# Optimization experiments

Hardware: AMD Instinct MI355X
Metric: run time of the kernel (lower is better)

## Reference

```python
import jax, jax.numpy as jnp
import numpy as np
import math

B, L, DIM, DEPTH, HEADS, DH, T, BUCKETS, MAXDIST = 256, 77, 768, 12, 12, 64, 1000, 32, 128
INNER = HEADS * DH            # 768
FF_IN = 4 * DIM               # 3072 (SwiGLU inner)
EPS = 1e-5


def rmsnorm(x, gamma):
    inv = jax.lax.rsqrt(jnp.sum(x * x, axis=-1, keepdims=True) + EPS)
    return x * inv * gamma * (DIM ** 0.5)


def rel_pos_bias(i, j, table):
    # table: [BUCKETS, HEADS] -> bias [HEADS, i, j]
    q_pos = jnp.arange(i)
    k_pos = jnp.arange(j)
    rel = k_pos[None, :] - q_pos[:, None]
    n = jnp.maximum(-rel, 0)
    max_exact = BUCKETS // 2
    is_small = n < max_exact
    nf = jnp.maximum(n, 1).astype(jnp.float32)
    val_large = max_exact + (jnp.log(nf / max_exact) / math.log(MAXDIST / max_exact) * (BUCKETS - max_exact)).astype(jnp.int32)
    val_large = jnp.minimum(val_large, BUCKETS - 1)
    bucket = jnp.where(is_small, n, val_large)
    return jnp.transpose(table[bucket], (2, 0, 1))  # h i j


def attention(x, mask, bias, gamma, Wq, Wkv, Wout, null_kv):
    b, n, _ = x.shape
    xn = rmsnorm(x, gamma)
    q = (xn @ Wq).reshape(b, n, HEADS, DH).transpose(0, 2, 1, 3)     # b h n d
    kv = xn @ Wkv                                                     # b n 2d (single head)
    k, v = kv[..., :DH], kv[..., DH:]
    nk = jnp.broadcast_to(null_kv[0], (b, 1, DH))
    nv = jnp.broadcast_to(null_kv[1], (b, 1, DH))
    k = jnp.concatenate([nk, k], axis=1)                              # b (n+1) d
    v = jnp.concatenate([nv, v], axis=1)
    sim = jnp.einsum('bhid,bjd->bhij', q * (DH ** -0.5), k) + bias[None]
    neg = -jnp.finfo(sim.dtype).max
    m = jnp.pad(mask, ((0, 0), (1, 0)), constant_values=True)         # null kv always visible
    sim = jnp.where(m[:, None, None, :], sim, neg)
    i, j = n, n + 1
    causal = jnp.arange(j)[None, :] > (jnp.arange(i)[:, None] + (j - i))
    sim = jnp.where(causal[None, None], neg, sim)
    attn = jax.nn.softmax(sim - jax.lax.stop_gradient(sim.max(axis=-1, keepdims=True)), axis=-1)
    out = jnp.einsum('bhij,bjd->bhid', attn, v)
    out = out.transpose(0, 2, 1, 3).reshape(b, n, INNER)
    return out @ Wout


def feedforward(x, gamma, W1, W2):
    h = rmsnorm(x, gamma) @ W1                                        # b n 2*FF_IN
    a, gate = h[..., :FF_IN], h[..., FF_IN:]
    return (a * jax.nn.silu(gate)) @ W2


def setup_inputs() -> dict:
    key = jax.random.key(0)
    ks = jax.random.split(key, 16)
    s = 0.02
    return {
        'image_embed': jax.random.normal(ks[0], (B, DIM), jnp.float32),
        'text_encodings': jax.random.normal(ks[1], (B, L, DIM), jnp.float32),
        'text_embed': jax.random.normal(ks[2], (B, DIM), jnp.float32),
        'time_emb_table': jax.random.normal(ks[3], (T, DIM), jnp.float32) * s,
        'learned_query': jax.random.normal(ks[4], (DIM,), jnp.float32),
        'rel_bias_table': jax.random.normal(ks[5], (BUCKETS, HEADS), jnp.float32) * s,
        'attn_gamma': jnp.ones((DEPTH, DIM), jnp.float32),
        'Wq': jax.random.normal(ks[6], (DEPTH, DIM, INNER), jnp.float32) * s,
        'Wkv': jax.random.normal(ks[7], (DEPTH, DIM, 2 * DH), jnp.float32) * s,
        'Wout': jax.random.normal(ks[8], (DEPTH, INNER, DIM), jnp.float32) * s,
        'null_kv': jax.random.normal(ks[9], (DEPTH, 2, DH), jnp.float32),
        'ff_gamma': jnp.ones((DEPTH, DIM), jnp.float32),
        'Wff1': jax.random.normal(ks[10], (DEPTH, DIM, 2 * FF_IN), jnp.float32) * s,
        'Wff2': jax.random.normal(ks[11], (DEPTH, FF_IN, DIM), jnp.float32) * s,
        'diffusion_timesteps': jax.random.randint(ks[12], (B,), 0, T),
        'mask': jnp.ones((B, L), dtype=bool),
    }


def reference(image_embed, text_encodings, text_embed, time_emb_table, learned_query,
              rel_bias_table, attn_gamma, Wq, Wkv, Wout, null_kv, ff_gamma, Wff1, Wff2,
              diffusion_timesteps, mask):
    b = image_embed.shape[0]
    # mask bookkeeping (matches torch forward); cond_drop_prob fixed at 1.0 -> keep all
    not_all = jnp.any(mask, axis=-1)
    m = jnp.concatenate([mask, not_all[:, None]], axis=1)
    m = jnp.pad(m, ((0, 0), (0, 2)), constant_values=True)            # [b, L+3]
    time_embed = time_emb_table[diffusion_timesteps][:, None, :]
    queries = jnp.broadcast_to(learned_query, (b, 1, DIM))
    tokens = jnp.concatenate([text_encodings, text_embed[:, None, :], time_embed, queries], axis=1)
    n = tokens.shape[1]
    bias = rel_pos_bias(n, n + 1, rel_bias_table)
    x = tokens
    for l in range(DEPTH):
        x = attention(x, m, bias, attn_gamma[l], Wq[l], Wkv[l], Wout[l], null_kv[l]) + x
        x = feedforward(x, ff_gamma[l], Wff1[l], Wff2[l]) + x
    return x[:, -1, :]
```

## Files before the change

### kernel.cpp

```cpp
#include <hip/hip_runtime.h>
#include <hip/hip_bf16.h>
#include <float.h>
#include <math.h>

#define NB 256
#define LTXT 77
#define DIM 768
#define DEPTH 12
#define HEADS 12
#define DH 64
#define NTOK 80
#define NKEY 81
#define NROWS (NB*NTOK)
#define FFH 3072
#define FF2C 6144
#define INNER 768
#define SROW 100

typedef __hip_bfloat16 bf16;
typedef __attribute__((ext_vector_type(8))) short short8;
typedef __attribute__((ext_vector_type(4))) float f32x4;

#define BARRIER() asm volatile("s_barrier" ::: "memory")
#define WAITV(n)  asm volatile("s_waitcnt vmcnt(" #n ")" ::: "memory")

__device__ __forceinline__ unsigned short f2bf(float f) {
    __hip_bfloat16 h = __float2bfloat16(f);
    return __builtin_bit_cast(unsigned short, h);
}

__global__ void build_tokens(const float* __restrict__ text_enc,
                             const float* __restrict__ text_emb,
                             const float* __restrict__ time_tab,
                             const float* __restrict__ lquery,
                             const int* __restrict__ tsteps,
                             float* __restrict__ x) {
    int idx = blockIdx.x * 256 + threadIdx.x;
    if (idx >= NROWS * DIM) return;
    int d = idx % DIM;
    int row = idx / DIM;
    int b = row / NTOK, p = row % NTOK;
    float v;
    if (p < LTXT)            v = text_enc[((size_t)b * LTXT + p) * DIM + d];
    else if (p == LTXT)      v = text_emb[(size_t)b * DIM + d];
    else if (p == LTXT + 1)  v = time_tab[(size_t)tsteps[b] * DIM + d];
    else                     v = lquery[d];
    x[idx] = v;
}

__global__ void build_biasR(const float* __restrict__ table, float* __restrict__ biasR) {
    int idx = blockIdx.x * 256 + threadIdx.x;
    if (idx >= HEADS * NTOK * 96) return;
    int kap = idx % 96;
    int i = (idx / 96) % NTOK;
    int h = idx / (96 * NTOK);
    float v;
    if ((kap < 80 && kap > i) || kap > 80) {
        v = -1e30f;
    } else {
        int j = (kap < 80) ? kap + 1 : 0;
        int rel = j - i;
        int n = rel < 0 ? -rel : 0;
        int bucket;
        if (n < 16) {
            bucket = n;
        } else {
            float val = logf((float)n / 16.0f) / logf(8.0f) * 16.0f;
            int vl = 16 + (int)val;
            bucket = vl < 31 ? vl : 31;
        }
        v = table[bucket * HEADS + h];
    }
    biasR[idx] = v;
}

__global__ __launch_bounds__(256) void convT(const float* __restrict__ W,
                                             bf16* __restrict__ WT,
                                             int K, int N) {
    __shared__ float t[32][33];
    int n0 = blockIdx.x * 32, k0 = blockIdx.y * 32;
    int tx = threadIdx.x & 31, ty = threadIdx.x >> 5;
    #pragma unroll
    for (int i = 0; i < 4; i++)
        t[ty + 8 * i][tx] = W[(size_t)(k0 + ty + 8 * i) * N + n0 + tx];
    __syncthreads();
    #pragma unroll
    for (int i = 0; i < 4; i++)
        WT[(size_t)(n0 + ty + 8 * i) * K + k0 + tx] = __float2bfloat16(t[tx][ty + 8 * i]);
}

__global__ __launch_bounds__(256) void rmsnorm_w(const float* __restrict__ x,
                                                 const float* __restrict__ gamma,
                                                 bf16* __restrict__ out) {
    int wave = blockIdx.x * 4 + (threadIdx.x >> 6);
    int lane = threadIdx.x & 63;
    float4 g0 = *(const float4*)&gamma[lane * 4];
    float4 g1 = *(const float4*)&gamma[lane * 4 + 256];
    float4 g2 = *(const float4*)&gamma[lane * 4 + 512];
    #pragma unroll 2
    for (int rr = 0; rr < 8; ++rr) {
        int row = wave * 8 + rr;
        const float* xr = x + (size_t)row * DIM + lane * 4;
        float4 v0 = *(const float4*)xr;
        float4 v1 = *(const float4*)(xr + 256);
        float4 v2 = *(const float4*)(xr + 512);
        float ss = v0.x*v0.x + v0.y*v0.y + v0.z*v0.z + v0.w*v0.w
                 + v1.x*v1.x + v1.y*v1.y + v1.z*v1.z + v1.w*v1.w
                 + v2.x*v2.x + v2.y*v2.y + v2.z*v2.z + v2.w*v2.w;
        #pragma unroll
        for (int o = 32; o > 0; o >>= 1) ss += __shfl_xor(ss, o);
        float inv = 27.712812921102035f / sqrtf(ss + 1e-5f);
        bf16* orow = out + (size_t)row * DIM + lane * 4;
        ushort4 w0 = { f2bf(v0.x*inv*g0.x), f2bf(v0.y*inv*g0.y), f2bf(v0.z*inv*g0.z), f2bf(v0.w*inv*g0.w) };
        ushort4 w1 = { f2bf(v1.x*inv*g1.x), f2bf(v1.y*inv*g1.y), f2bf(v1.z*inv*g1.z), f2bf(v1.w*inv*g1.w) };
        ushort4 w2 = { f2bf(v2.x*inv*g2.x), f2bf(v2.y*inv*g2.y), f2bf(v2.z*inv*g2.z), f2bf(v2.w*inv*g2.w) };
        *(ushort4*)(orow)       = w0;
        *(ushort4*)(orow + 256) = w1;
        *(ushort4*)(orow + 512) = w2;
    }
}


#define GSTAGE_N(nld, lds, base, b0, ld, kk0)                                  \
    _Pragma("unroll")                                                          \
    for (int r_ = 0; r_ < (nld); ++r_) {                                       \
        int idx_ = r_ * 256 + t;                                               \
        int row_ = idx_ >> 3, c_ = idx_ & 7;                                   \
        int cs_ = c_ ^ (row_ & 7);                                             \
        __builtin_amdgcn_global_load_lds(                                      \
            (const __attribute__((address_space(1))) unsigned int*)            \
                &base[(size_t)(b0 + row_) * ld + (kk0) + cs_ * 8],             \
            (__attribute__((address_space(3))) unsigned int*)&lds[idx_ * 8],   \
            16, 0, 0);                                                         \
    }

#define FRAG_READ(dst, lds, base_row, kk)                                      \
    _Pragma("unroll")                                                          \
    for (int q_ = 0; q_ < 4; ++q_) {                                           \
        int row_ = (base_row) + q_ * 16 + fr;                                  \
        int ch_ = ((((kk) << 2) + kb) ^ (row_ & 7));                           \
        dst[q_] = *(const short8*)&lds[row_ * 64 + ch_ * 8];                   \
    }

#define FRAG_READ2(dst, lds, base_row, kk)                                     \
    _Pragma("unroll")                                                          \
    for (int q_ = 0; q_ < 2; ++q_) {                                           \
        int row_ = (base_row) + q_ * 16 + fr;                                  \
        int ch_ = ((((kk) << 2) + kb) ^ (row_ & 7));                           \
        dst[q_] = *(const short8*)&lds[row_ * 64 + ch_ * 8];                   \
    }

template<int EPI>
__global__ __launch_bounds__(256, 2) void gemm_bt(const bf16* __restrict__ A,
                                                  const bf16* __restrict__ BT,
                                                  float* __restrict__ C,
                                                  int N, int K) {
    __shared__ __align__(16) short As[2 * 128 * 64];
    __shared__ __align__(16) short Bs[2 * 128 * 64];
    const int t = threadIdx.x;
    const int lane = t & 63;
    const int wid = t >> 6;
    const int wr = wid >> 1, wc = wid & 1;
    const int fr = lane & 15;
    const int kb = lane >> 4;
    const int row0 = blockIdx.y * 128, col0 = blockIdx.x * 128;

    f32x4 acc[4][4] = {};
    const int NKT = K >> 6;

    GSTAGE_N(4, As, A, row0, K, 0)
    GSTAGE_N(4, Bs, BT, col0, K, 0)

    for (int kt = 0; kt < NKT; ++kt) {
        const short* curA = As + (kt & 1) * (128 * 64);
        const short* curB = Bs + (kt & 1) * (128 * 64);
        if (kt + 1 < NKT) {
            short* nxtA = As + ((kt + 1) & 1) * (128 * 64);
            short* nxtB = Bs + ((kt + 1) & 1) * (128 * 64);
            int k0n = (kt + 1) << 6;
            GSTAGE_N(4, nxtA, A, row0, K, k0n)
            GSTAGE_N(4, nxtB, BT, col0, K, k0n)
            WAITV(8);
        } else {
            WAITV(0);
        }
        BARRIER();
        #pragma unroll
        for (int kk = 0; kk < 2; ++kk) {
            short8 af[4], bv[4];
            FRAG_READ(af, curA, wr * 64, kk)
            FRAG_READ(bv, curB, wc * 64, kk)
            __builtin_amdgcn_s_setprio(1);
            #pragma unroll
            for (int i = 0; i < 4; ++i)
                #pragma unroll
                for (int j = 0; j < 4; ++j)
                    acc[i][j] = __builtin_amdgcn_mfma_f32_16x16x32_bf16(af[i], bv[j], acc[i][j], 0, 0, 0);
            __builtin_amdgcn_s_setprio(0);
        }
        BARRIER();
    }

    #pragma unroll
    for (int i = 0; i < 4; ++i) {
        #pragma unroll
        for (int j = 0; j < 4; ++j) {
            int row = row0 + wr * 64 + i * 16 + kb * 4;
            int col = col0 + wc * 64 + j * 16 + fr;
            #pragma unroll
            for (int r = 0; r < 4; ++r) {
                size_t o = (size_t)(row + r) * N + col;
                if (EPI == 1)      C[o] += acc[i][j][r];
                else               ((bf16*)C)[o] = __float2bfloat16(acc[i][j][r]);
            }
        }
    }
}

__global__ __launch_bounds__(256, 2) void gemm_kv(const bf16* __restrict__ A,
                                                  const bf16* __restrict__ BT,
                                                  bf16* __restrict__ kout,
                                                  bf16* __restrict__ vT) {
    __shared__ __align__(16) short As[2 * 128 * 64];
    __shared__ __align__(16) short Bs[2 * 128 * 64];
    const int t = threadIdx.x;
    const int lane = t & 63;
    const int wid = t >> 6;
    const int wr = wid >> 1, wc = wid & 1;
    const int fr = lane & 15;
    const int kb = lane >> 4;
    const int row0 = blockIdx.y * 128;
    const int K = DIM;

    f32x4 acc[4][4] = {};
    const int NKT = DIM >> 6;

    GSTAGE_N(4, As, A, row0, K, 0)
    GSTAGE_N(4, Bs, BT, 0, K, 0)

    for (int kt = 0; kt < NKT; ++kt) {
        const short* curA = As + (kt & 1) * (128 * 64);
        const short* curB = Bs + (kt & 1) * (128 * 64);
        if (kt + 1 < NKT) {
            short* nxtA = As + ((kt + 1) & 1) * (128 * 64);
            short* nxtB = Bs + ((kt + 1) & 1) * (128 * 64);
            int k0n = (kt + 1) << 6;
            GSTAGE_N(4, nxtA, A, row0, K, k0n)
            GSTAGE_N(4, nxtB, BT, 0, K, k0n)
            WAITV(8);
        } else {
            WAITV(0);
        }
        BARRIER();
        #pragma unroll
        for (int kk = 0; kk < 2; ++kk) {
            short8 af[4], bv[4];
            FRAG_READ(af, curA, wr * 64, kk)
            FRAG_READ(bv, curB, wc * 64, kk)
            __builtin_amdgcn_s_setprio(1);
            #pragma unroll
            for (int i = 0; i < 4; ++i)
                #pragma unroll
                for (int j = 0; j < 4; ++j)
                    acc[i][j] = __builtin_amdgcn_mfma_f32_16x16x32_bf16(af[i], bv[j], acc[i][j], 0, 0, 0);
            __builtin_amdgcn_s_setprio(0);
        }
        BARRIER();
    }

    #pragma unroll
    for (int i = 0; i < 4; ++i) {
        #pragma unroll
        for (int j = 0; j < 4; ++j) {
            int row = row0 + wr * 64 + i * 16 + kb * 4;
            int col = wc * 64 + j * 16 + fr;
            #pragma unroll
            for (int r = 0; r < 4; ++r) {
                int rg = row + r;
                float v = acc[i][j][r];
                if (wc == 0) {
                    kout[(size_t)rg * 64 + col] = __float2bfloat16(v);
                } else {
                    int bb = rg / NTOK, ii = rg - bb * NTOK;
                    vT[((size_t)bb * 64 + (col - 64)) * NTOK + ii] = __float2bfloat16(v);
                }
            }
        }
    }
}

__global__ __launch_bounds__(256) void attn_mfma(const bf16* __restrict__ qb,
                                                 const bf16* __restrict__ kbuf,
                                                 const bf16* __restrict__ vT,
                                                 const float* __restrict__ nullkv,
                                                 const float* __restrict__ biasR,
                                                 bf16* __restrict__ attnb) {
    const int b = blockIdx.x / HEADS;
    const int h = blockIdx.x % HEADS;
    __shared__ __align__(16) short Ks[96 * 64];
    __shared__ __align__(16) short Vt[64 * 128];
    __shared__ __align__(16) float Sls[80 * SROW];
    char* Sb = (char*)Sls;
    const int t = threadIdx.x;
    const int lane = t & 63;
    const int wid = t >> 6;
    const int g = lane >> 4;
    const int fr = lane & 15;

    for (int c = t; c < 768; c += 256) {
        int row = c >> 3, ch = c & 7;
        short8 v;
        if (row < NTOK) {
            v = *(const short8*)&kbuf[((size_t)(b * NTOK + row)) * 64 + ch * 8];
        } else if (row == NTOK) {
            #pragma unroll
            for (int e = 0; e < 8; ++e) v[e] = (short)f2bf(nullkv[ch * 8 + e]);
        } else {
            v = short8{0,0,0,0,0,0,0,0};
        }
        *(short8*)((char*)Ks + row * 128 + ((ch ^ (row & 7)) << 4)) = v;
    }
    for (int c = t; c < 1024; c += 256) {
        int d = c >> 4, ch = c & 15;
        if (ch >= 12) continue;
        short8 v;
        if (ch < 10) {
            v = *(const short8*)&vT[((size_t)b * 64 + d) * NTOK + ch * 8];
        } else if (ch == 10) {
            v = short8{0,0,0,0,0,0,0,0};
            v[0] = (short)f2bf(nullkv[64 + d]);
        } else {
            v = short8{0,0,0,0,0,0,0,0};
        }
        *(short8*)((char*)Vt + d * 256 + ((ch ^ (d & 7)) << 4)) = v;
    }
    __syncthreads();

    const bf16* qbase = qb + ((size_t)(b * NTOK)) * INNER + h * DH;
    for (int s = 0; s < 8; ++s) {
        int tt = wid + 4 * s;
        if (tt >= 30) break;
        int m = tt / 6, n = tt - 6 * m;
        f32x4 acc = {};
        #pragma unroll
        for (int kk = 0; kk < 2; ++kk) {
            short8 a = *(const short8*)&qbase[(size_t)(m * 16 + fr) * INNER + kk * 32 + g * 8];
            int krow = n * 16 + fr;
            short8 kf = *(const short8*)((const char*)Ks + krow * 128 + ((((kk << 2) + g) ^ (krow & 7)) << 4));
            acc = __builtin_amdgcn_mfma_f32_16x16x32_bf16(a, kf, acc, 0, 0, 0);
        }
        int i0 = m * 16 + g * 4;
        int kap = n * 16 + fr;
        const float* bR = biasR + ((size_t)h * NTOK + i0) * 96 + kap;
        #pragma unroll
        for (int r = 0; r < 4; ++r)
            Sls[(i0 + r) * SROW + kap] = acc[r] * 0.125f + bR[r * 96];
    }
    __syncthreads();

    for (int rr = 0; rr < 20; ++rr) {
        int row = wid + 4 * rr;
        const float* Srow = Sls + row * SROW;
        float s0 = Srow[lane];
        float s1v = Srow[64 + (lane & 31)];
        float mx = fmaxf(s0, s1v);
        #pragma unroll
        for (int o = 32; o > 0; o >>= 1) mx = fmaxf(mx, __shfl_xor(mx, o));
        float e0 = __expf(s0 - mx);
        float e1 = (lane < 32) ? __expf(s1v - mx) : 0.0f;
        float sum = e0 + e1;
        #pragma unroll
        for (int o = 32; o > 0; o >>= 1) sum += __shfl_xor(sum, o);
        float inv = 1.0f / sum;
        *(unsigned short*)(Sb + row * (SROW * 4) + lane * 2) = f2bf(e0 * inv);
        if (lane < 32)
            *(unsigned short*)(Sb + row * (SROW * 4) + 128 + lane * 2) = f2bf(e1 * inv);
    }
    __syncthreads();

    for (int s = 0; s < 5; ++s) {
        int tt = wid + 4 * s;
        int m = tt >> 2, n = tt & 3;
        f32x4 acc = {};
        #pragma unroll
        for (int kc = 0; kc < 3; ++kc) {
            short8 p = *(const short8*)(Sb + (m * 16 + fr) * (SROW * 4) + kc * 64 + g * 16);
            int drow = n * 16 + fr;
            short8 vv = *(const short8*)((const char*)Vt + drow * 256 + ((((kc << 2) + g) ^ (drow & 7)) << 4));
            acc = __builtin_amdgcn_mfma_f32_16x16x32_bf16(p, vv, acc, 0, 0, 0);
        }
        int i0 = m * 16 + g * 4;
        int d = n * 16 + fr;
        #pragma unroll
        for (int r = 0; r < 4; ++r)
            attnb[((size_t)(b * NTOK) + i0 + r) * INNER + h * DH + d] = __float2bfloat16(acc[r]);
    }
}

__global__ __launch_bounds__(256, 2) void gemm_ff1(const bf16* __restrict__ A,
                                                   const bf16* __restrict__ W1T,
                                                   bf16* __restrict__ act) {
    __shared__ __align__(16) short As[2 * 128 * 64];
    __shared__ __align__(16) short Bs1[2 * 64 * 64];
    __shared__ __align__(16) short Bs2[2 * 64 * 64];
    const int t = threadIdx.x;
    const int lane = t & 63;
    const int wid = t >> 6;
    const int wr = wid >> 1, wc = wid & 1;
    const int fr = lane & 15;
    const int kb = lane >> 4;
    const int row0 = blockIdx.y * 128, col0 = blockIdx.x * 64;
    const int K = DIM;
    const bf16* B1 = W1T;
    const bf16* B2 = W1T + (size_t)FFH * DIM;

    f32x4 acc1[4][2] = {}, acc2[4][2] = {};
    const int NKT = DIM >> 6;

    GSTAGE_N(4, As, A, row0, K, 0)
    GSTAGE_N(2, Bs1, B1, col0, K, 0)
    GSTAGE_N(2, Bs2, B2, col0, K, 0)

    for (int kt = 0; kt < NKT; ++kt) {
        const short* curA  = As  + (kt & 1) * (128 * 64);
        const short* curB1 = Bs1 + (kt & 1) * (64 * 64);
        const short* curB2 = Bs2 + (kt & 1) * (64 * 64);
        if (kt + 1 < NKT) {
            short* nxtA  = As  + ((kt + 1) & 1) * (128 * 64);
            short* nxtB1 = Bs1 + ((kt + 1) & 1) * (64 * 64);
            short* nxtB2 = Bs2 + ((kt + 1) & 1) * (64 * 64);
            int k0n = (kt + 1) << 6;
            GSTAGE_N(4, nxtA, A, row0, K, k0n)
            GSTAGE_N(2, nxtB1, B1, col0, K, k0n)
            GSTAGE_N(2, nxtB2, B2, col0, K, k0n)
            WAITV(8);
        } else {
            WAITV(0);
        }
        BARRIER();
        #pragma unroll
        for (int kk = 0; kk < 2; ++kk) {
            short8 af[4], b1v[2], b2v[2];
            FRAG_READ(af, curA, wr * 64, kk)
            FRAG_READ2(b1v, curB1, wc * 32, kk)
            FRAG_READ2(b2v, curB2, wc * 32, kk)
            __builtin_amdgcn_s_setprio(1);
            #pragma unroll
            for (int i = 0; i < 4; ++i)
                #pragma unroll
                for (int j = 0; j < 2; ++j) {
                    acc1[i][j] = __builtin_amdgcn_mfma_f32_16x16x32_bf16(af[i], b1v[j], acc1[i][j], 0, 0, 0);
                    acc2[i][j] = __builtin_amdgcn_mfma_f32_16x16x32_bf16(af[i], b2v[j], acc2[i][j], 0, 0, 0);
                }
            __builtin_amdgcn_s_setprio(0);
        }
        BARRIER();
    }

    #pragma unroll
    for (int i = 0; i < 4; ++i) {
        #pragma unroll
        for (int j = 0; j < 2; ++j) {
            int row = row0 + wr * 64 + i * 16 + kb * 4;
            int col = col0 + wc * 32 + j * 16 + fr;
            #pragma unroll
            for (int r = 0; r < 4; ++r) {
                float a = acc1[i][j][r];
                float gt = acc2[i][j][r];
                float s = a * gt / (1.0f + __expf(-gt));
                act[(size_t)(row + r) * FFH + col] = __float2bfloat16(s);
            }
        }
    }
}

__global__ void extract(const float* __restrict__ x, float* __restrict__ out) {
    int idx = blockIdx.x * 256 + threadIdx.x;
    if (idx >= NB * DIM) return;
    int b = idx / DIM, d = idx % DIM;
    out[idx] = x[((size_t)(b * NTOK + NTOK - 1)) * DIM + d];
}

extern "C" void kernel_launch(void* const* d_in, const int* in_sizes, int n_in,
                              void* d_out, int out_size, void* d_ws, size_t ws_size,
                              hipStream_t stream) {
    (void)in_sizes; (void)n_in; (void)out_size; (void)ws_size;
    const float* text_enc = (const float*)d_in[1];
    const float* text_emb = (const float*)d_in[2];
    const float* time_tab = (const float*)d_in[3];
    const float* lquery   = (const float*)d_in[4];
    const float* rel_tab  = (const float*)d_in[5];
    const float* attn_g   = (const float*)d_in[6];
    const float* Wq       = (const float*)d_in[7];
    const float* Wkv      = (const float*)d_in[8];
    const float* Wout     = (const float*)d_in[9];
    const float* null_kv  = (const float*)d_in[10];
    const float* ff_g     = (const float*)d_in[11];
    const float* Wff1     = (const float*)d_in[12];
    const float* Wff2     = (const float*)d_in[13];
    const int*   tsteps   = (const int*)d_in[14];

    char* ws = (char*)d_ws;
    float* x     = (float*)(ws);
    bf16*  xn    = (bf16*)(ws + 62914560);
    bf16*  attnb = xn;
    char*  U     = ws + 94371840;
    bf16*  qb    = (bf16*)U;
    bf16*  kbuf  = (bf16*)(U + 31457280);
    bf16*  vT    = (bf16*)(U + 34078720);
    bf16*  act   = (bf16*)U;
    float* biasR = (float*)(ws + 220200960);
    bf16*  WqT   = (bf16*)(ws + 220569600);
    bf16*  WkvT  = (bf16*)(ws + 221749248);
    bf16*  WoutT = (bf16*)(ws + 221945856);
    bf16*  Wff1T = (bf16*)(ws + 223125504);
    bf16*  Wff2T = (bf16*)(ws + 232562688);

    build_tokens<<<(NROWS * DIM + 255) / 256, 256, 0, stream>>>(text_enc, text_emb, time_tab, lquery, tsteps, x);
    build_biasR<<<(HEADS * NTOK * 96 + 255) / 256, 256, 0, stream>>>(rel_tab, biasR);

    for (int l = 0; l < DEPTH; l++) {
        convT<<<dim3(INNER / 32, DIM / 32), 256, 0, stream>>>(Wq   + (size_t)l * DIM * INNER,  WqT,   DIM,   INNER);
        convT<<<dim3((2 * DH) / 32, DIM / 32), 256, 0, stream>>>(Wkv + (size_t)l * DIM * 2 * DH, WkvT, DIM, 2 * DH);
        convT<<<dim3(DIM / 32, INNER / 32), 256, 0, stream>>>(Wout + (size_t)l * INNER * DIM,  WoutT, INNER, DIM);
        convT<<<dim3(FF2C / 32, DIM / 32), 256, 0, stream>>>(Wff1 + (size_t)l * DIM * FF2C,    Wff1T, DIM,   FF2C);
        convT<<<dim3(DIM / 32, FFH / 32), 256, 0, stream>>>(Wff2  + (size_t)l * FFH * DIM,     Wff2T, FFH,   DIM);

        rmsnorm_w<<<NROWS / (8 * 4), 256, 0, stream>>>(x, attn_g + (size_t)l * DIM, xn);
        gemm_bt<2><<<dim3(INNER / 128, NROWS / 128), 256, 0, stream>>>(xn, WqT, (float*)qb, INNER, DIM);
        gemm_kv<<<dim3(1, NROWS / 128), 256, 0, stream>>>(xn, WkvT, kbuf, vT);
        attn_mfma<<<NB * HEADS, 256, 0, stream>>>(qb, kbuf, vT, null_kv + (size_t)l * 2 * DH, biasR, attnb);
        gemm_bt<1><<<dim3(DIM / 128, NROWS / 128), 256, 0, stream>>>(attnb, WoutT, x, DIM, INNER);

        rmsnorm_w<<<NROWS / (8 * 4), 256, 0, stream>>>(x, ff_g + (size_t)l * DIM, xn);
        gemm_ff1<<<dim3(FFH / 64, NROWS / 128), 256, 0, stream>>>(xn, Wff1T, act);
        gemm_bt<1><<<dim3(DIM / 128, NROWS / 128), 256, 0, stream>>>(act, Wff2T, x, DIM, FFH);
    }

    extract<<<(NB * DIM + 255) / 256, 256, 0, stream>>>(x, (float*)d_out);
}
```

Before: 7.894 ms.

## Skip non-final-token work in last layer, fuse QKV GEMM and weight conversions

In the last layer, only the final token's row is needed after attention, so the output projection, FF norm and both FF GEMMs run on just those 256 rows using strided leading dimensions. The Q and KV projections are merged into one GEMM over a concatenated transposed weight, and the five per-layer weight transposes become one launch. This removes about a twelfth of the FF and output-projection compute plus several launches. The cost is extra stride parameters and special-case code paths.

```diff
diff --git a/kernel.cpp b/kernel.cpp
--- a/kernel.cpp
+++ b/kernel.cpp
@@ -74,19 +74,34 @@
     biasR[idx] = v;
 }
 
-__global__ __launch_bounds__(256) void convT(const float* __restrict__ W,
-                                             bf16* __restrict__ WT,
-                                             int K, int N) {
-    __shared__ float t[32][33];
-    int n0 = blockIdx.x * 32, k0 = blockIdx.y * 32;
+__global__ __launch_bounds__(256) void convT_all(const float* __restrict__ Wq,
+                                                 const float* __restrict__ Wkv,
+                                                 const float* __restrict__ Wout,
+                                                 const float* __restrict__ Wff1,
+                                                 const float* __restrict__ Wff2,
+                                                 bf16* __restrict__ WqkvT,
+                                                 bf16* __restrict__ WoutT,
+                                                 bf16* __restrict__ Wff1T,
+                                                 bf16* __restrict__ Wff2T) {
+    int bid = blockIdx.x;
+    const float* W; bf16* WT; int K, N, local;
+    if (bid < 576)       { W = Wq;   WT = WqkvT;             K = 768;  N = 768;  local = bid; }
+    else if (bid < 672)  { W = Wkv;  WT = WqkvT + 768 * 768; K = 768;  N = 128;  local = bid - 576; }
+    else if (bid < 1248) { W = Wout; WT = WoutT;             K = 768;  N = 768;  local = bid - 672; }
+    else if (bid < 5856) { W = Wff1; WT = Wff1T;             K = 768;  N = 6144; local = bid - 1248; }
+    else                 { W = Wff2; WT = Wff2T;             K = 3072; N = 768;  local = bid - 5856; }
+    int nblk = N / 32;
+    int n0 = (local % nblk) * 32, k0 = (local / nblk) * 32;
+
+    __shared__ float tt[32][33];
     int tx = threadIdx.x & 31, ty = threadIdx.x >> 5;
     #pragma unroll
     for (int i = 0; i < 4; i++)
-        t[ty + 8 * i][tx] = W[(size_t)(k0 + ty + 8 * i) * N + n0 + tx];
+        tt[ty + 8 * i][tx] = W[(size_t)(k0 + ty + 8 * i) * N + n0 + tx];
     __syncthreads();
     #pragma unroll
     for (int i = 0; i < 4; i++)
-        WT[(size_t)(n0 + ty + 8 * i) * K + k0 + tx] = __float2bfloat16(t[tx][ty + 8 * i]);
+        WT[(size_t)(n0 + ty + 8 * i) * K + k0 + tx] = __float2bfloat16(tt[tx][ty + 8 * i]);
 }
 
 __global__ __launch_bounds__(256) void rmsnorm_w(const float* __restrict__ x,
@@ -120,6 +135,37 @@
     }
 }
 
+__global__ __launch_bounds__(256) void rmsnorm_last(const float* __restrict__ x,
+                                                    const float* __restrict__ gamma,
+                                                    bf16* __restrict__ out) {
+    int wave = blockIdx.x * 4 + (threadIdx.x >> 6);
+    int lane = threadIdx.x & 63;
+    float4 g0 = *(const float4*)&gamma[lane * 4];
+    float4 g1 = *(const float4*)&gamma[lane * 4 + 256];
+    float4 g2 = *(const float4*)&gamma[lane * 4 + 512];
+    #pragma unroll 2
+    for (int rr = 0; rr < 8; ++rr) {
+        int row = wave * 8 + rr;
+        const float* xr = x + ((size_t)row * NTOK + 79) * DIM + lane * 4;
+        float4 v0 = *(const float4*)xr;
+        float4 v1 = *(const float4*)(xr + 256);
+        float4 v2 = *(const float4*)(xr + 512);
+        float ss = v0.x*v0.x + v0.y*v0.y + v0.z*v0.z + v0.w*v0.w
+                 + v1.x*v1.x + v1.y*v1.y + v1.z*v1.z + v1.w*v1.w
+                 + v2.x*v2.x + v2.y*v2.y + v2.z*v2.z + v2.w*v2.w;
+        #pragma unroll
+        for (int o = 32; o > 0; o >>= 1) ss += __shfl_xor(ss, o);
+        float inv = 27.712812921102035f / sqrtf(ss + 1e-5f);
+        bf16* orow = out + (size_t)row * DIM + lane * 4;
+        ushort4 w0 = { f2bf(v0.x*inv*g0.x), f2bf(v0.y*inv*g0.y), f2bf(v0.z*inv*g0.z), f2bf(v0.w*inv*g0.w) };
+        ushort4 w1 = { f2bf(v1.x*inv*g1.x), f2bf(v1.y*inv*g1.y), f2bf(v1.z*inv*g1.z), f2bf(v1.w*inv*g1.w) };
+        ushort4 w2 = { f2bf(v2.x*inv*g2.x), f2bf(v2.y*inv*g2.y), f2bf(v2.z*inv*g2.z), f2bf(v2.w*inv*g2.w) };
+        *(ushort4*)(orow)       = w0;
+        *(ushort4*)(orow + 256) = w1;
+        *(ushort4*)(orow + 512) = w2;
+    }
+}
+
 
 #define GSTAGE_N(nld, lds, base, b0, ld, kk0)                                  \
     _Pragma("unroll")                                                          \
@@ -129,7 +175,7 @@
         int cs_ = c_ ^ (row_ & 7);                                             \
         __builtin_amdgcn_global_load_lds(                                      \
             (const __attribute__((address_space(1))) unsigned int*)            \
-                &base[(size_t)(b0 + row_) * ld + (kk0) + cs_ * 8],             \
+                &base[(size_t)(b0 + row_) * (ld) + (kk0) + cs_ * 8],           \
             (__attribute__((address_space(3))) unsigned int*)&lds[idx_ * 8],   \
             16, 0, 0);                                                         \
     }
@@ -154,7 +200,7 @@
 __global__ __launch_bounds__(256, 2) void gemm_bt(const bf16* __restrict__ A,
                                                   const bf16* __restrict__ BT,
                                                   float* __restrict__ C,
-                                                  int N, int K) {
+                                                  int N, int K, int lda, int ldc) {
     __shared__ __align__(16) short As[2 * 128 * 64];
     __shared__ __align__(16) short Bs[2 * 128 * 64];
     const int t = threadIdx.x;
@@ -167,6 +213,73 @@
 
     f32x4 acc[4][4] = {};
     const int NKT = K >> 6;
+
+    GSTAGE_N(4, As, A, row0, lda, 0)
+    GSTAGE_N(4, Bs, BT, col0, K, 0)
+
+    for (int kt = 0; kt < NKT; ++kt) {
+        const short* curA = As + (kt & 1) * (128 * 64);
+        const short* curB = Bs + (kt & 1) * (128 * 64);
+        if (kt + 1 < NKT) {
+            short* nxtA = As + ((kt + 1) & 1) * (128 * 64);
+            short* nxtB = Bs + ((kt + 1) & 1) * (128 * 64);
+            int k0n = (kt + 1) << 6;
+            GSTAGE_N(4, nxtA, A, row0, lda, k0n)
+            GSTAGE_N(4, nxtB, BT, col0, K, k0n)
+            WAITV(8);
+        } else {
+            WAITV(0);
+        }
+        BARRIER();
+        #pragma unroll
+        for (int kk = 0; kk < 2; ++kk) {
+            short8 af[4], bv[4];
+            FRAG_READ(af, curA, wr * 64, kk)
+            FRAG_READ(bv, curB, wc * 64, kk)
+            __builtin_amdgcn_s_setprio(1);
+            #pragma unroll
+            for (int i = 0; i < 4; ++i)
+                #pragma unroll
+                for (int j = 0; j < 4; ++j)
+                    acc[i][j] = __builtin_amdgcn_mfma_f32_16x16x32_bf16(af[i], bv[j], acc[i][j], 0, 0, 0);
+            __builtin_amdgcn_s_setprio(0);
+        }
+        BARRIER();
+    }
+
+    #pragma unroll
+    for (int i = 0; i < 4; ++i) {
+        #pragma unroll
+        for (int j = 0; j < 4; ++j) {
+            int row = row0 + wr * 64 + i * 16 + kb * 4;
+            int col = col0 + wc * 64 + j * 16 + fr;
+            #pragma unroll
+            for (int r = 0; r < 4; ++r) {
+                size_t o = (size_t)(row + r) * ldc + col;
+                C[o] += acc[i][j][r];
+            }
+        }
+    }
+}
+
+__global__ __launch_bounds__(256, 2) void gemm_qkv(const bf16* __restrict__ A,
+                                                   const bf16* __restrict__ BT,
+                                                   bf16* __restrict__ qb,
+                                                   bf16* __restrict__ kout,
+                                                   bf16* __restrict__ vT) {
+    __shared__ __align__(16) short As[2 * 128 * 64];
+    __shared__ __align__(16) short Bs[2 * 128 * 64];
+    const int t = threadIdx.x;
+    const int lane = t & 63;
+    const int wid = t >> 6;
+    const int wr = wid >> 1, wc = wid & 1;
+    const int fr = lane & 15;
+    const int kb = lane >> 4;
+    const int row0 = blockIdx.y * 128, col0 = blockIdx.x * 128;
+    const int K = DIM;
+
+    f32x4 acc[4][4] = {};
+    const int NKT = DIM >> 6;
 
     GSTAGE_N(4, As, A, row0, K, 0)
     GSTAGE_N(4, Bs, BT, col0, K, 0)
@@ -201,52 +314,77 @@
         BARRIER();
     }
 
-    #pragma unroll
-    for (int i = 0; i < 4; ++i) {
-        #pragma unroll
-        for (int j = 0; j < 4; ++j) {
-            int row = row0 + wr * 64 + i * 16 + kb * 4;
-            int col = col0 + wc * 64 + j * 16 + fr;
-            #pragma unroll
-            for (int r = 0; r < 4; ++r) {
-                size_t o = (size_t)(row + r) * N + col;
-                if (EPI == 1)      C[o] += acc[i][j][r];
-                else               ((bf16*)C)[o] = __float2bfloat16(acc[i][j][r]);
+    if (col0 < 768) {
+        #pragma unroll
+        for (int i = 0; i < 4; ++i) {
+            #pragma unroll
+            for (int j = 0; j < 4; ++j) {
+                int row = row0 + wr * 64 + i * 16 + kb * 4;
+                int col = col0 + wc * 64 + j * 16 + fr;
+                #pragma unroll
+                for (int r = 0; r < 4; ++r)
+                    qb[(size_t)(row + r) * INNER + col] = __float2bfloat16(acc[i][j][r]);
             }
         }
-    }
-}
-
-__global__ __launch_bounds__(256, 2) void gemm_kv(const bf16* __restrict__ A,
-                                                  const bf16* __restrict__ BT,
-                                                  bf16* __restrict__ kout,
-                                                  bf16* __restrict__ vT) {
+    } else {
+        #pragma unroll
+        for (int i = 0; i < 4; ++i) {
+            #pragma unroll
+            for (int j = 0; j < 4; ++j) {
+                int row = row0 + wr * 64 + i * 16 + kb * 4;
+                int col = wc * 64 + j * 16 + fr;
+                #pragma unroll
+                for (int r = 0; r < 4; ++r) {
+                    int rg = row + r;
+                    float v = acc[i][j][r];
+                    if (wc == 0) {
+                        kout[(size_t)rg * 64 + col] = __float2bfloat16(v);
+                    } else {
+                        int bb = rg / NTOK, ii = rg - bb * NTOK;
+                        vT[((size_t)bb * 64 + (col - 64)) * NTOK + ii] = __float2bfloat16(v);
+                    }
+                }
+            }
+        }
+    }
+}
+
+__global__ __launch_bounds__(256, 2) void gemm_ff1(const bf16* __restrict__ A,
+                                                   const bf16* __restrict__ W1T,
+                                                   bf16* __restrict__ act) {
     __shared__ __align__(16) short As[2 * 128 * 64];
-    __shared__ __align__(16) short Bs[2 * 128 * 64];
+    __shared__ __align__(16) short Bs1[2 * 64 * 64];
+    __shared__ __align__(16) short Bs2[2 * 64 * 64];
     const int t = threadIdx.x;
     const int lane = t & 63;
     const int wid = t >> 6;
     const int wr = wid >> 1, wc = wid & 1;
     const int fr = lane & 15;
     const int kb = lane >> 4;
-    const int row0 = blockIdx.y * 128;
+    const int row0 = blockIdx.y * 128, col0 = blockIdx.x * 64;
     const int K = DIM;
-
-    f32x4 acc[4][4] = {};
+    const bf16* B1 = W1T;
+    const bf16* B2 = W1T + (size_t)FFH * DIM;
+
+    f32x4 acc1[4][2] = {}, acc2[4][2] = {};
     const int NKT = DIM >> 6;
 
     GSTAGE_N(4, As, A, row0, K, 0)
-    GSTAGE_N(4, Bs, BT, 0, K, 0)
+    GSTAGE_N(2, Bs1, B1, col0, K, 0)
+    GSTAGE_N(2, Bs2, B2, col0, K, 0)
 
     for (int kt = 0; kt < NKT; ++kt) {
-        const short* curA = As + (kt & 1) * (128 * 64);
-        const short* curB = Bs + (kt & 1) * (128 * 64);
+        const short* curA  = As  + (kt & 1) * (128 * 64);
+        const short* curB1 = Bs1 + (kt & 1) * (64 * 64);
+        const short* curB2 = Bs2 + (kt & 1) * (64 * 64);
         if (kt + 1 < NKT) {
-            short* nxtA = As + ((kt + 1) & 1) * (128 * 64);
-            short* nxtB = Bs + ((kt + 1) & 1) * (128 * 64);
+            short* nxtA  = As  + ((kt + 1) & 1) * (128 * 64);
+            short* nxtB1 = Bs1 + ((kt + 1) & 1) * (64 * 64);
+            short* nxtB2 = Bs2 + ((kt + 1) & 1) * (64 * 64);
             int k0n = (kt + 1) << 6;
             GSTAGE_N(4, nxtA, A, row0, K, k0n)
-            GSTAGE_N(4, nxtB, BT, 0, K, k0n)
+            GSTAGE_N(2, nxtB1, B1, col0, K, k0n)
+            GSTAGE_N(2, nxtB2, B2, col0, K, k0n)
             WAITV(8);
         } else {
             WAITV(0);
@@ -254,15 +392,18 @@
         BARRIER();
         #pragma unroll
         for (int kk = 0; kk < 2; ++kk) {
-            short8 af[4], bv[4];
+            short8 af[4], b1v[2], b2v[2];
             FRAG_READ(af, curA, wr * 64, kk)
-            FRAG_READ(bv, curB, wc * 64, kk)
+            FRAG_READ2(b1v, curB1, wc * 32, kk)
+            FRAG_READ2(b2v, curB2, wc * 32, kk)
             __builtin_amdgcn_s_setprio(1);
             #pragma unroll
             for (int i = 0; i < 4; ++i)
                 #pragma unroll
-                for (int j = 0; j < 4; ++j)
-                    acc[i][j] = __builtin_amdgcn_mfma_f32_16x16x32_bf16(af[i], bv[j], acc[i][j], 0, 0, 0);
+                for (int j = 0; j < 2; ++j) {
+                    acc1[i][j] = __builtin_amdgcn_mfma_f32_16x16x32_bf16(af[i], b1v[j], acc1[i][j], 0, 0, 0);
+                    acc2[i][j] = __builtin_amdgcn_mfma_f32_16x16x32_bf16(af[i], b2v[j], acc2[i][j], 0, 0, 0);
+                }
             __builtin_amdgcn_s_setprio(0);
         }
         BARRIER();
@@ -271,19 +412,15 @@
     #pragma unroll
     for (int i = 0; i < 4; ++i) {
         #pragma unroll
-        for (int j = 0; j < 4; ++j) {
+        for (int j = 0; j < 2; ++j) {
             int row = row0 + wr * 64 + i * 16 + kb * 4;
-            int col = wc * 64 + j * 16 + fr;
+            int col = col0 + wc * 32 + j * 16 + fr;
             #pragma unroll
             for (int r = 0; r < 4; ++r) {
-                int rg = row + r;
-                float v = acc[i][j][r];
-                if (wc == 0) {
-                    kout[(size_t)rg * 64 + col] = __float2bfloat16(v);
-                } else {
-                    int bb = rg / NTOK, ii = rg - bb * NTOK;
-                    vT[((size_t)bb * 64 + (col - 64)) * NTOK + ii] = __float2bfloat16(v);
-                }
+                float a = acc1[i][j][r];
+                float gt = acc2[i][j][r];
+                float s = a * gt / (1.0f + __expf(-gt));
+                act[(size_t)(row + r) * FFH + col] = __float2bfloat16(s);
             }
         }
     }
@@ -394,83 +531,6 @@
         #pragma unroll
         for (int r = 0; r < 4; ++r)
             attnb[((size_t)(b * NTOK) + i0 + r) * INNER + h * DH + d] = __float2bfloat16(acc[r]);
-    }
-}
-
-__global__ __launch_bounds__(256, 2) void gemm_ff1(const bf16* __restrict__ A,
-                                                   const bf16* __restrict__ W1T,
-                                                   bf16* __restrict__ act) {
-    __shared__ __align__(16) short As[2 * 128 * 64];
-    __shared__ __align__(16) short Bs1[2 * 64 * 64];
-    __shared__ __align__(16) short Bs2[2 * 64 * 64];
-    const int t = threadIdx.x;
-    const int lane = t & 63;
-    const int wid = t >> 6;
-    const int wr = wid >> 1, wc = wid & 1;
-    const int fr = lane & 15;
-    const int kb = lane >> 4;
-    const int row0 = blockIdx.y * 128, col0 = blockIdx.x * 64;
-    const int K = DIM;
-    const bf16* B1 = W1T;
-    const bf16* B2 = W1T + (size_t)FFH * DIM;
-
-    f32x4 acc1[4][2] = {}, acc2[4][2] = {};
-    const int NKT = DIM >> 6;
-
-    GSTAGE_N(4, As, A, row0, K, 0)
-    GSTAGE_N(2, Bs1, B1, col0, K, 0)
-    GSTAGE_N(2, Bs2, B2, col0, K, 0)
-
-    for (int kt = 0; kt < NKT; ++kt) {
-        const short* curA  = As  + (kt & 1) * (128 * 64);
-        const short* curB1 = Bs1 + (kt & 1) * (64 * 64);
-        const short* curB2 = Bs2 + (kt & 1) * (64 * 64);
-        if (kt + 1 < NKT) {
-            short* nxtA  = As  + ((kt + 1) & 1) * (128 * 64);
-            short* nxtB1 = Bs1 + ((kt + 1) & 1) * (64 * 64);
-            short* nxtB2 = Bs2 + ((kt + 1) & 1) * (64 * 64);
-            int k0n = (kt + 1) << 6;
-            GSTAGE_N(4, nxtA, A, row0, K, k0n)
-            GSTAGE_N(2, nxtB1, B1, col0, K, k0n)
-            GSTAGE_N(2, nxtB2, B2, col0, K, k0n)
-            WAITV(8);
-        } else {
-            WAITV(0);
-        }
-        BARRIER();
-        #pragma unroll
-        for (int kk = 0; kk < 2; ++kk) {
-            short8 af[4], b1v[2], b2v[2];
-            FRAG_READ(af, curA, wr * 64, kk)
-            FRAG_READ2(b1v, curB1, wc * 32, kk)
-            FRAG_READ2(b2v, curB2, wc * 32, kk)
-            __builtin_amdgcn_s_setprio(1);
-            #pragma unroll
-            for (int i = 0; i < 4; ++i)
-                #pragma unroll
-                for (int j = 0; j < 2; ++j) {
-                    acc1[i][j] = __builtin_amdgcn_mfma_f32_16x16x32_bf16(af[i], b1v[j], acc1[i][j], 0, 0, 0);
-                    acc2[i][j] = __builtin_amdgcn_mfma_f32_16x16x32_bf16(af[i], b2v[j], acc2[i][j], 0, 0, 0);
-                }
-            __builtin_amdgcn_s_setprio(0);
-        }
-        BARRIER();
-    }
-
-    #pragma unroll
-    for (int i = 0; i < 4; ++i) {
-        #pragma unroll
-        for (int j = 0; j < 2; ++j) {
-            int row = row0 + wr * 64 + i * 16 + kb * 4;
-            int col = col0 + wc * 32 + j * 16 + fr;
-            #pragma unroll
-            for (int r = 0; r < 4; ++r) {
-                float a = acc1[i][j][r];
-                float gt = acc2[i][j][r];
-                float s = a * gt / (1.0f + __expf(-gt));
-                act[(size_t)(row + r) * FFH + col] = __float2bfloat16(s);
-            }
-        }
     }
 }
 
@@ -510,8 +570,7 @@
     bf16*  vT    = (bf16*)(U + 34078720);
     bf16*  act   = (bf16*)U;
     float* biasR = (float*)(ws + 220200960);
-    bf16*  WqT   = (bf16*)(ws + 220569600);
-    bf16*  WkvT  = (bf16*)(ws + 221749248);
+    bf16*  WqkvT = (bf16*)(ws + 220569600);
     bf16*  WoutT = (bf16*)(ws + 221945856);
     bf16*  Wff1T = (bf16*)(ws + 223125504);
     bf16*  Wff2T = (bf16*)(ws + 232562688);
@@ -520,21 +579,32 @@
     build_biasR<<<(HEADS * NTOK * 96 + 255) / 256, 256, 0, stream>>>(rel_tab, biasR);
 
     for (int l = 0; l < DEPTH; l++) {
-        convT<<<dim3(INNER / 32, DIM / 32), 256, 0, stream>>>(Wq   + (size_t)l * DIM * INNER,  WqT,   DIM,   INNER);
-        convT<<<dim3((2 * DH) / 32, DIM / 32), 256, 0, stream>>>(Wkv + (size_t)l * DIM * 2 * DH, WkvT, DIM, 2 * DH);
-        convT<<<dim3(DIM / 32, INNER / 32), 256, 0, stream>>>(Wout + (size_t)l * INNER * DIM,  WoutT, INNER, DIM);
-        convT<<<dim3(FF2C / 32, DIM / 32), 256, 0, stream>>>(Wff1 + (size_t)l * DIM * FF2C,    Wff1T, DIM,   FF2C);
-        convT<<<dim3(DIM / 32, FFH / 32), 256, 0, stream>>>(Wff2  + (size_t)l * FFH * DIM,     Wff2T, FFH,   DIM);
-
-        rmsnorm_w<<<NROWS / (8 * 4), 256, 0, stream>>>(x, attn_g + (size_t)l * DIM, xn);
-        gemm_bt<2><<<dim3(INNER / 128, NROWS / 128), 256, 0, stream>>>(xn, WqT, (float*)qb, INNER, DIM);
-        gemm_kv<<<dim3(1, NROWS / 128), 256, 0, stream>>>(xn, WkvT, kbuf, vT);
+        convT_all<<<8160, 256, 0, stream>>>(Wq   + (size_t)l * DIM * INNER,
+                                            Wkv  + (size_t)l * DIM * 2 * DH,
+                                            Wout + (size_t)l * INNER * DIM,
+                                            Wff1 + (size_t)l * DIM * FF2C,
+                                            Wff2 + (size_t)l * FFH * DIM,
+                                            WqkvT, WoutT, Wff1T, Wff2T);
+
+        rmsnorm_w<<<NROWS / 32, 256, 0, stream>>>(x, attn_g + (size_t)l * DIM, xn);
+        gemm_qkv<<<dim3(7, NROWS / 128), 256, 0, stream>>>(xn, WqkvT, qb, kbuf, vT);
         attn_mfma<<<NB * HEADS, 256, 0, stream>>>(qb, kbuf, vT, null_kv + (size_t)l * 2 * DH, biasR, attnb);
-        gemm_bt<1><<<dim3(DIM / 128, NROWS / 128), 256, 0, stream>>>(attnb, WoutT, x, DIM, INNER);
-
-        rmsnorm_w<<<NROWS / (8 * 4), 256, 0, stream>>>(x, ff_g + (size_t)l * DIM, xn);
-        gemm_ff1<<<dim3(FFH / 64, NROWS / 128), 256, 0, stream>>>(xn, Wff1T, act);
-        gemm_bt<1><<<dim3(DIM / 128, NROWS / 128), 256, 0, stream>>>(act, Wff2T, x, DIM, FFH);
+
+        if (l < DEPTH - 1) {
+            gemm_bt<1><<<dim3(DIM / 128, NROWS / 128), 256, 0, stream>>>(attnb, WoutT, x, DIM, INNER, INNER, DIM);
+            rmsnorm_w<<<NROWS / 32, 256, 0, stream>>>(x, ff_g + (size_t)l * DIM, xn);
+            gemm_ff1<<<dim3(FFH / 64, NROWS / 128), 256, 0, stream>>>(xn, Wff1T, act);
+            gemm_bt<1><<<dim3(DIM / 128, NROWS / 128), 256, 0, stream>>>(act, Wff2T, x, DIM, FFH, FFH, DIM);
+        } else {
+            gemm_bt<1><<<dim3(DIM / 128, 2), 256, 0, stream>>>(
+                attnb + (size_t)79 * INNER, WoutT, x + (size_t)79 * DIM,
+                DIM, INNER, NTOK * INNER, NTOK * DIM);
+            rmsnorm_last<<<8, 256, 0, stream>>>(x, ff_g + (size_t)l * DIM, xn);
+            gemm_ff1<<<dim3(FFH / 64, 2), 256, 0, stream>>>(xn, Wff1T, act);
+            gemm_bt<1><<<dim3(DIM / 128, 2), 256, 0, stream>>>(
+                act, Wff2T, x + (size_t)79 * DIM,
+                DIM, FFH, FFH, NTOK * DIM);
+        }
     }
 
     extract<<<(NB * DIM + 255) / 256, 256, 0, stream>>>(x, (float*)d_out);
```

Result: faster. 7.427 ms (-5.9%).
